# Kernel tuning notes

Hardware: AMD Instinct MI355X
Metric: run time of the kernel (lower is better)

## Reference

```python
import jax, jax.numpy as jnp
import numpy as np

B, L, C, H, FF = 2, 2048, 1024, 16, 4096
HD = C // H
SCALE = HD ** -0.5
EPS = 1e-5


def _ln(x, g, b):
    m = jnp.mean(x, axis=-1, keepdims=True)
    v = jnp.mean((x - m) ** 2, axis=-1, keepdims=True)
    return (x - m) * jax.lax.rsqrt(v + EPS) * g + b


def setup_inputs() -> dict:
    key = jax.random.key(0)
    ks = jax.random.split(key, 12)
    s = lambda fan_in: 1.0 / np.sqrt(fan_in)
    return {
        "x": jax.random.normal(ks[0], (B, L, C), jnp.float32),
        "freq_diff": jax.random.normal(ks[1], (B, L), jnp.float32),
        "qkv_w": jax.random.normal(ks[2], (C, 3 * C), jnp.float32) * s(C),
        "qkv_b": jnp.zeros((3 * C,), jnp.float32),
        "fp_w1": jax.random.normal(ks[3], (1, C), jnp.float32),
        "fp_b1": jnp.zeros((C,), jnp.float32),
        "fp_ln_g": jnp.ones((C,), jnp.float32),
        "fp_ln_b": jnp.zeros((C,), jnp.float32),
        "fp_w2": jax.random.normal(ks[4], (C, C), jnp.float32) * s(C),
        "fp_b2": jnp.zeros((C,), jnp.float32),
        "wq_w": jax.random.normal(ks[5], (HD, HD), jnp.float32) * s(HD),
        "wq_b": jnp.zeros((HD,), jnp.float32),
        "wk_w": jax.random.normal(ks[6], (HD, HD), jnp.float32) * s(HD),
        "wk_b": jnp.zeros((HD,), jnp.float32),
        "out_w": jax.random.normal(ks[7], (C, C), jnp.float32) * s(C),
        "out_b": jnp.zeros((C,), jnp.float32),
        "n1_g": jnp.ones((C,), jnp.float32),
        "n1_b": jnp.zeros((C,), jnp.float32),
        "n2_g": jnp.ones((C,), jnp.float32),
        "n2_b": jnp.zeros((C,), jnp.float32),
        "mlp_w1": jax.random.normal(ks[8], (C, FF), jnp.float32) * s(C),
        "mlp_b1": jnp.zeros((FF,), jnp.float32),
        "mlp_w2": jax.random.normal(ks[9], (FF, C), jnp.float32) * s(FF),
        "mlp_b2": jnp.zeros((C,), jnp.float32),
        "freq_scale": jnp.ones((1,), jnp.float32),
    }


def reference(x, freq_diff, qkv_w, qkv_b, fp_w1, fp_b1, fp_ln_g, fp_ln_b,
              fp_w2, fp_b2, wq_w, wq_b, wk_w, wk_b, out_w, out_b,
              n1_g, n1_b, n2_g, n2_b, mlp_w1, mlp_b1, mlp_w2, mlp_b2,
              freq_scale):
    shortcut = x
    xn = _ln(x, n1_g, n1_b)
    qkv = (xn @ qkv_w + qkv_b).reshape(B, L, 3, H, HD)
    qkv = jnp.transpose(qkv, (2, 0, 3, 1, 4))  # [3,B,H,L,HD]
    q, k, v = qkv[0], qkv[1], qkv[2]

    # frequency bias: MLP on scalar freq_diff -> per-head bias vectors
    fb = freq_diff[..., None] @ fp_w1 + fp_b1          # [B,L,C]
    fb = jax.nn.gelu(_ln(fb, fp_ln_g, fp_ln_b), approximate=False)
    fb = fb @ fp_w2 + fp_b2                            # [B,L,C]
    fb = jnp.transpose(fb.reshape(B, L, H, HD), (0, 2, 1, 3))  # [B,H,L,HD]
    qb = fb @ wq_w + wq_b
    kb = fb @ wk_w + wk_b
    freq_attn_bias = jnp.einsum('bhqd,bhkd->bhqk', qb, kb)

    attn = jnp.einsum('bhqd,bhkd->bhqk', q, k) * SCALE
    attn = attn + freq_scale[0] * freq_attn_bias
    attn = jax.nn.softmax(attn, axis=-1)
    o = jnp.einsum('bhqk,bhkd->bhqd', attn, v)
    o = jnp.transpose(o, (0, 2, 1, 3)).reshape(B, L, C)
    x = shortcut + (o @ out_w + out_b)

    xn2 = _ln(x, n2_g, n2_b)
    h = jax.nn.gelu(xn2 @ mlp_w1 + mlp_b1, approximate=False)
    x = x + (h @ mlp_w2 + mlp_b2)
    return x
```

## Files before the change

kernel.cpp:

```cpp
#include <hip/hip_runtime.h>
#include <math.h>


typedef __bf16 bf16;
typedef float f32x4 __attribute__((ext_vector_type(4)));
typedef bf16 bf16x8 __attribute__((ext_vector_type(8)));
typedef bf16 bf16x4 __attribute__((ext_vector_type(4)));

#define DEVINL __device__ __forceinline__

DEVINL void async_load16(const void* g, void* l) {
  __builtin_amdgcn_global_load_lds(
      (const __attribute__((address_space(1))) unsigned int*)g,
      (__attribute__((address_space(3))) unsigned int*)l, 16, 0, 0);
}

DEVINL f32x4 mfma16(bf16x8 a, bf16x8 b, f32x4 c) {
  return __builtin_amdgcn_mfma_f32_16x16x32_bf16(a, b, c, 0, 0, 0);
}

DEVINL float gelu_exact(float v) {
  return 0.5f * v * (1.0f + erff(v * 0.70710678118654752f));
}

DEVINL void block_reduce2(float& a, float& b, float* red, int tid) {
#pragma unroll
  for (int off = 32; off >= 1; off >>= 1) {
    a += __shfl_xor(a, off);
    b += __shfl_xor(b, off);
  }
  int w = tid >> 6;
  if ((tid & 63) == 0) { red[2 * w] = a; red[2 * w + 1] = b; }
  __syncthreads();
  a = red[0] + red[2] + red[4] + red[6];
  b = red[1] + red[3] + red[5] + red[7];
  __syncthreads();
}

__global__ __launch_bounds__(256) void transpose_cast(
    const float* __restrict__ W, bf16* __restrict__ Wt, int K, int N) {
  __shared__ float tile[32][33];
  int n0 = blockIdx.x * 32, k0 = blockIdx.y * 32;
  int tx = threadIdx.x & 31, ty = threadIdx.x >> 5;
#pragma unroll
  for (int r = 0; r < 4; ++r)
    tile[ty + r * 8][tx] = W[(size_t)(k0 + ty + r * 8) * N + n0 + tx];
  __syncthreads();
#pragma unroll
  for (int r = 0; r < 4; ++r)
    Wt[(size_t)(n0 + ty + r * 8) * K + k0 + tx] = (bf16)tile[tx][ty + r * 8];
}

__global__ __launch_bounds__(256) void prec_qk(
    const float* __restrict__ fp_w2, const float* __restrict__ fp_b2,
    const float* __restrict__ wq_w, const float* __restrict__ wq_b,
    const float* __restrict__ wk_w, const float* __restrict__ wk_b,
    bf16* __restrict__ wqk2t, float* __restrict__ bqk) {
  __shared__ float Wl[64 * 64];
  __shared__ float Al[64 * 128];
  const int id = blockIdx.x;
  const int sel = id >> 7, h = (id >> 3) & 15, ck = id & 7;
  const int t = threadIdx.x;
  const float* wsel = sel ? wk_w : wq_w;
#pragma unroll
  for (int i = 0; i < 4; ++i)
    ((float4*)Wl)[i * 256 + t] = ((const float4*)wsel)[i * 256 + t];
  const int c0 = ck * 128, off = h * 64;
#pragma unroll
  for (int it = 0; it < 8; ++it) {
    int idx = it * 256 + t;
    int rr = idx >> 4, c4 = idx & 15;
    float4 v = *(const float4*)(fp_w2 + (size_t)(c0 + rr) * 1024 + off + c4 * 4);
    float vv[4] = {v.x, v.y, v.z, v.w};
#pragma unroll
    for (int k = 0; k < 4; ++k) {
      int i2 = c4 * 4 + k;
      Al[i2 * 128 + (rr ^ (i2 & 31))] = vv[k];
    }
  }
  __syncthreads();
  const int cr = t & 127, jh = (t >> 7) * 32;
  float acc[32];
#pragma unroll
  for (int j = 0; j < 32; ++j) acc[j] = 0.f;
  for (int i = 0; i < 64; ++i) {
    float a = Al[i * 128 + (cr ^ (i & 31))];
    const float4* wrow = (const float4*)(Wl + i * 64 + jh);
#pragma unroll
    for (int j4 = 0; j4 < 8; ++j4) {
      float4 wv = wrow[j4];
      acc[j4 * 4 + 0] += a * wv.x;
      acc[j4 * 4 + 1] += a * wv.y;
      acc[j4 * 4 + 2] += a * wv.z;
      acc[j4 * 4 + 3] += a * wv.w;
    }
  }
  const int nbase = sel * 1024 + off + jh;
#pragma unroll
  for (int j = 0; j < 32; ++j)
    wqk2t[(size_t)(nbase + j) * 1024 + c0 + cr] = (bf16)acc[j];
  if (ck == 0 && t < 64) {
    float s = 0.f;
    for (int i = 0; i < 64; ++i) s += fp_b2[off + i] * Wl[i * 64 + t];
    bqk[sel * 1024 + off + t] = s + (sel ? wk_b[t] : wq_b[t]);
  }
}

__global__ __launch_bounds__(256) void ln1_kernel(
    const float* __restrict__ x, const float* __restrict__ fd,
    const float* __restrict__ g1, const float* __restrict__ b1,
    const float* __restrict__ fw1, const float* __restrict__ fb1,
    const float* __restrict__ flg, const float* __restrict__ flb,
    bf16* __restrict__ xn, bf16* __restrict__ gout) {
  __shared__ float red[8];
  int tok = blockIdx.x, t = threadIdx.x;
  float4 xv = ((const float4*)(x + (size_t)tok * 1024))[t];
  float s = xv.x + xv.y + xv.z + xv.w;
  float ss = xv.x * xv.x + xv.y * xv.y + xv.z * xv.z + xv.w * xv.w;
  block_reduce2(s, ss, red, t);
  float mean = s * (1.0f / 1024.0f);
  float rsig = rsqrtf(ss * (1.0f / 1024.0f) - mean * mean + 1e-5f);
  float4 g4 = ((const float4*)g1)[t], b4 = ((const float4*)b1)[t];
  bf16x4 o;
  o[0] = (bf16)((xv.x - mean) * rsig * g4.x + b4.x);
  o[1] = (bf16)((xv.y - mean) * rsig * g4.y + b4.y);
  o[2] = (bf16)((xv.z - mean) * rsig * g4.z + b4.z);
  o[3] = (bf16)((xv.w - mean) * rsig * g4.w + b4.w);
  ((bf16x4*)xn)[(size_t)tok * 256 + t] = o;

  float dv = fd[tok];
  float4 w4 = ((const float4*)fw1)[t], c4 = ((const float4*)fb1)[t];
  float f0 = dv * w4.x + c4.x, f1 = dv * w4.y + c4.y;
  float f2 = dv * w4.z + c4.z, f3 = dv * w4.w + c4.w;
  s = f0 + f1 + f2 + f3;
  ss = f0 * f0 + f1 * f1 + f2 * f2 + f3 * f3;
  block_reduce2(s, ss, red, t);
  mean = s * (1.0f / 1024.0f);
  rsig = rsqrtf(ss * (1.0f / 1024.0f) - mean * mean + 1e-5f);
  float4 lg = ((const float4*)flg)[t], lb = ((const float4*)flb)[t];
  bf16x4 q;
  q[0] = (bf16)gelu_exact((f0 - mean) * rsig * lg.x + lb.x);
  q[1] = (bf16)gelu_exact((f1 - mean) * rsig * lg.y + lb.y);
  q[2] = (bf16)gelu_exact((f2 - mean) * rsig * lg.z + lb.z);
  q[3] = (bf16)gelu_exact((f3 - mean) * rsig * lg.w + lb.w);
  ((bf16x4*)gout)[(size_t)tok * 256 + t] = q;
}

__global__ __launch_bounds__(256) void ln_kernel(
    const float* __restrict__ xin, const float* __restrict__ g,
    const float* __restrict__ b, bf16* __restrict__ xout) {
  __shared__ float red[8];
  int tok = blockIdx.x, t = threadIdx.x;
  float4 xv = ((const float4*)(xin + (size_t)tok * 1024))[t];
  float s = xv.x + xv.y + xv.z + xv.w;
  float ss = xv.x * xv.x + xv.y * xv.y + xv.z * xv.z + xv.w * xv.w;
  block_reduce2(s, ss, red, t);
  float mean = s * (1.0f / 1024.0f);
  float rsig = rsqrtf(ss * (1.0f / 1024.0f) - mean * mean + 1e-5f);
  float4 g4 = ((const float4*)g)[t], b4 = ((const float4*)b)[t];
  bf16x4 o;
  o[0] = (bf16)((xv.x - mean) * rsig * g4.x + b4.x);
  o[1] = (bf16)((xv.y - mean) * rsig * g4.y + b4.y);
  o[2] = (bf16)((xv.z - mean) * rsig * g4.z + b4.z);
  o[3] = (bf16)((xv.w - mean) * rsig * g4.w + b4.w);
  ((bf16x4*)xout)[(size_t)tok * 256 + t] = o;
}

template <class Epi>
__global__ __launch_bounds__(256) void gemm_bf16_k(
    const bf16* __restrict__ A, const bf16* __restrict__ Bt,
    int M, int N, int K, Epi epi) {
  __shared__ bf16 As[2][128 * 32];
  __shared__ bf16 Bs[2][128 * 32];
  const int tid = threadIdx.x;
  const int lane = tid & 63, w = tid >> 6;
  const int quad = lane >> 4, lm = lane & 15;
  const int wm = w >> 1, wn = w & 1;
  const int m0 = blockIdx.y * 128, n0 = blockIdx.x * 128;

  f32x4 acc[4][4];
#pragma unroll
  for (int i = 0; i < 4; ++i)
#pragma unroll
    for (int j = 0; j < 4; ++j) {
      acc[i][j][0] = 0.f; acc[i][j][1] = 0.f; acc[i][j][2] = 0.f; acc[i][j][3] = 0.f;
    }

  const bf16* Ag = A + (size_t)m0 * K;
  const bf16* Bg = Bt + (size_t)n0 * K;

  auto stage = [&](int k0, int buf) {
#pragma unroll
    for (int i = 0; i < 2; ++i) {
      int ch = i * 256 + tid, r = ch >> 2, c = ch & 3;
      async_load16(Ag + (size_t)r * K + k0 + c * 8,
                   (char*)As[buf] + (i * 256 + w * 64) * 16);
      async_load16(Bg + (size_t)r * K + k0 + c * 8,
                   (char*)Bs[buf] + (i * 256 + w * 64) * 16);
    }
  };

  stage(0, 0);
  const int nk = K >> 5;
  for (int ki = 0; ki < nk; ++ki) {
    __syncthreads();
    if (ki + 1 < nk) stage((ki + 1) << 5, (ki + 1) & 1);
    const bf16* Ac = As[ki & 1];
    const bf16* Bc = Bs[ki & 1];
    bf16x8 af[4], bfv[4];
#pragma unroll
    for (int mi = 0; mi < 4; ++mi)
      af[mi] = *(const bf16x8*)(Ac + (wm * 64 + mi * 16 + lm) * 32 + quad * 8);
#pragma unroll
    for (int ni = 0; ni < 4; ++ni)
      bfv[ni] = *(const bf16x8*)(Bc + (wn * 64 + ni * 16 + lm) * 32 + quad * 8);
#pragma unroll
    for (int mi = 0; mi < 4; ++mi)
#pragma unroll
      for (int ni = 0; ni < 4; ++ni)
        acc[mi][ni] = mfma16(af[mi], bfv[ni], acc[mi][ni]);
  }

#pragma unroll
  for (int mi = 0; mi < 4; ++mi)
#pragma unroll
    for (int ni = 0; ni < 4; ++ni)
      epi(m0 + wm * 64 + mi * 16 + quad * 4, n0 + wn * 64 + ni * 16 + lm, acc[mi][ni]);
}

__global__ __launch_bounds__(256) void gemm_mlp2_part(
    const bf16* __restrict__ A, const bf16* __restrict__ Bt,
    float* __restrict__ part) {
  __shared__ bf16 As[2][128 * 32];
  __shared__ bf16 Bs[2][128 * 32];
  const int tid = threadIdx.x;
  const int lane = tid & 63, w = tid >> 6;
  const int quad = lane >> 4, lm = lane & 15;
  const int wm = w >> 1, wn = w & 1;
  const int id = blockIdx.x;
  const int kz = id & 3;
  const int n0 = ((id >> 2) & 7) * 128;
  const int m0 = (id >> 5) * 128;

  f32x4 acc[4][4];
#pragma unroll
  for (int i = 0; i < 4; ++i)
#pragma unroll
    for (int j = 0; j < 4; ++j) {
      acc[i][j][0] = 0.f; acc[i][j][1] = 0.f; acc[i][j][2] = 0.f; acc[i][j][3] = 0.f;
    }

  const bf16* Ag = A + (size_t)m0 * 4096 + kz * 1024;
  const bf16* Bg = Bt + (size_t)n0 * 4096 + kz * 1024;

  auto stage = [&](int k0, int buf) {
#pragma unroll
    for (int i = 0; i < 2; ++i) {
      int ch = i * 256 + tid, r = ch >> 2, c = ch & 3;
      async_load16(Ag + (size_t)r * 4096 + k0 + c * 8,
                   (char*)As[buf] + (i * 256 + w * 64) * 16);
      async_load16(Bg + (size_t)r * 4096 + k0 + c * 8,
                   (char*)Bs[buf] + (i * 256 + w * 64) * 16);
    }
  };

  stage(0, 0);
  for (int ki = 0; ki < 32; ++ki) {
    __syncthreads();
    if (ki + 1 < 32) stage((ki + 1) << 5, (ki + 1) & 1);
    const bf16* Ac = As[ki & 1];
    const bf16* Bc = Bs[ki & 1];
    bf16x8 af[4], bfv[4];
#pragma unroll
    for (int mi = 0; mi < 4; ++mi)
      af[mi] = *(const bf16x8*)(Ac + (wm * 64 + mi * 16 + lm) * 32 + quad * 8);
#pragma unroll
    for (int ni = 0; ni < 4; ++ni)
      bfv[ni] = *(const bf16x8*)(Bc + (wn * 64 + ni * 16 + lm) * 32 + quad * 8);
#pragma unroll
    for (int mi = 0; mi < 4; ++mi)
#pragma unroll
      for (int ni = 0; ni < 4; ++ni)
        acc[mi][ni] = mfma16(af[mi], bfv[ni], acc[mi][ni]);
  }

  float* dst = part + (size_t)kz * 4096 * 1024;
#pragma unroll
  for (int mi = 0; mi < 4; ++mi)
#pragma unroll
    for (int ni = 0; ni < 4; ++ni) {
      int row = m0 + wm * 64 + mi * 16 + quad * 4;
      int col = n0 + wn * 64 + ni * 16 + lm;
#pragma unroll
      for (int r = 0; r < 4; ++r)
        dst[(size_t)(row + r) * 1024 + col] = acc[mi][ni][r];
    }
}

__global__ __launch_bounds__(256) void reduce_mlp2(
    const float* __restrict__ part, float* __restrict__ out) {
  size_t i = (size_t)blockIdx.x * 256 + threadIdx.x;
  const float4* p = (const float4*)part;
  float4 o = ((const float4*)out)[i];
  const size_t S = (size_t)4096 * 256;
  float4 a = p[i], b = p[i + S], c = p[i + 2 * S], d = p[i + 3 * S];
  o.x += a.x + b.x + c.x + d.x;
  o.y += a.y + b.y + c.y + d.y;
  o.z += a.z + b.z + c.z + d.z;
  o.w += a.w + b.w + c.w + d.w;
  ((float4*)out)[i] = o;
}

struct EpiQKV {
  const float* __restrict__ bias;
  bf16 *Qc, *Kc, *Vt;
  DEVINL void operator()(int row, int col, f32x4 v) const {
    int b = row >> 11, l = row & 2047;
    float bia = bias[col];
    if (col < 1024) {
      int h = col >> 6, d = col & 63;
      bf16* p = Qc + (size_t)(((b << 4) + h) * 2048 + l) * 128 + d;
#pragma unroll
      for (int r = 0; r < 4; ++r) p[r * 128] = (bf16)((v[r] + bia) * 0.125f);
    } else if (col < 2048) {
      int c2 = col - 1024, h = c2 >> 6, d = c2 & 63;
      bf16* p = Kc + (size_t)(((b << 4) + h) * 2048 + l) * 128 + d;
#pragma unroll
      for (int r = 0; r < 4; ++r) p[r * 128] = (bf16)(v[r] + bia);
    } else {
      int c2 = col - 2048, h = c2 >> 6, d = c2 & 63;
      bf16x4 pk;
#pragma unroll
      for (int r = 0; r < 4; ++r) pk[r] = (bf16)(v[r] + bia);
      *(bf16x4*)(Vt + (size_t)(((b << 4) + h) * 64 + d) * 2048 + l) = pk;
    }
  }
};

struct EpiQBKB {
  const float* __restrict__ bias;
  const float* __restrict__ fs;
  bf16 *Qc, *Kc;
  DEVINL void operator()(int row, int col, f32x4 v) const {
    int b = row >> 11, l = row & 2047;
    float bia = bias[col];
    if (col < 1024) {
      int h = col >> 6, d = col & 63;
      float sc = fs[0];
      bf16* p = Qc + (size_t)(((b << 4) + h) * 2048 + l) * 128 + 64 + d;
#pragma unroll
      for (int r = 0; r < 4; ++r) p[r * 128] = (bf16)((v[r] + bia) * sc);
    } else {
      int c2 = col - 1024, h = c2 >> 6, d = c2 & 63;
      bf16* p = Kc + (size_t)(((b << 4) + h) * 2048 + l) * 128 + 64 + d;
#pragma unroll
      for (int r = 0; r < 4; ++r) p[r * 128] = (bf16)(v[r] + bia);
    }
  }
};

struct EpiOut {
  const float* __restrict__ bias;
  const float* __restrict__ x;
  const float* __restrict__ b2;
  float* x1;
  float* out0;
  DEVINL void operator()(int row, int col, f32x4 v) const {
    float bia = bias[col];
    float b2v = b2[col];
#pragma unroll
    for (int r = 0; r < 4; ++r) {
      size_t idx = (size_t)(row + r) * 1024 + col;
      float xv = x[idx] + v[r] + bia;
      x1[idx] = xv;
      out0[idx] = xv + b2v;
    }
  }
};

struct EpiMLP1 {
  const float* __restrict__ bias;
  bf16* hbf;
  DEVINL void operator()(int row, int col, f32x4 v) const {
    float bia = bias[col];
#pragma unroll
    for (int r = 0; r < 4; ++r)
      hbf[(size_t)(row + r) * 4096 + col] = (bf16)gelu_exact(v[r] + bia);
  }
};

__global__ __launch_bounds__(256, 2) void flash_kernel(
    const bf16* __restrict__ Qc, const bf16* __restrict__ Kcp,
    const bf16* __restrict__ Vt, bf16* __restrict__ Obf) {
  __shared__ bf16 KsA[64 * 128];
  __shared__ bf16 KsB[64 * 128];
  __shared__ bf16 VsA[64 * 64];
  __shared__ bf16 VsB[64 * 64];
  __shared__ bf16 Ps[128 * 64];

  const int tid = threadIdx.x, lane = tid & 63, w = tid >> 6;
  const int quad = lane >> 4, lm = lane & 15;
  const int id = blockIdx.x;
  const int bh = id & 31, qt = id >> 5;
  const int b = bh >> 4, h = bh & 15;

  const bf16* Qg = Qc + ((size_t)bh * 2048 + qt * 128) * 128;
#pragma unroll
  for (int i = 0; i < 8; ++i) {
    int ch = i * 256 + tid, r = ch >> 4, cs = ch & 15, c = cs ^ (r & 7);
    char* dst = (r < 64) ? (char*)KsA + (i * 256 + w * 64) * 16
                         : (char*)KsB + ((i - 4) * 256 + w * 64) * 16;
    async_load16(Qg + (size_t)r * 128 + c * 8, dst);
  }
  __syncthreads();
  bf16x8 qf[2][4];
#pragma unroll
  for (int mi = 0; mi < 2; ++mi) {
    int r = w * 32 + mi * 16 + lm;
    const bf16* base = (r < 64) ? KsA : KsB;
#pragma unroll
    for (int ks = 0; ks < 4; ++ks) {
      int pos = (ks * 4 + quad) ^ (r & 7);
      qf[mi][ks] = *(const bf16x8*)(base + (r & 63) * 128 + pos * 8);
    }
  }
  __syncthreads();

  float m_run[2], l_run[2];
  f32x4 o_acc[2][4];
#pragma unroll
  for (int mi = 0; mi < 2; ++mi) { m_run[mi] = -3.0e38f; l_run[mi] = 0.f; }
#pragma unroll
  for (int mi = 0; mi < 2; ++mi)
#pragma unroll
    for (int nf = 0; nf < 4; ++nf) {
      o_acc[mi][nf][0] = 0.f; o_acc[mi][nf][1] = 0.f;
      o_acc[mi][nf][2] = 0.f; o_acc[mi][nf][3] = 0.f;
    }

  const bf16* Kg0 = Kcp + (size_t)bh * 2048 * 128;
  const bf16* Vg0 = Vt + (size_t)bh * 64 * 2048;

  auto stage = [&](int kv, bf16* Kdst, bf16* Vdst) {
    const bf16* Kg = Kg0 + (size_t)kv * 64 * 128;
#pragma unroll
    for (int i = 0; i < 4; ++i) {
      int ch = i * 256 + tid, key = ch >> 4, c = (ch & 15) ^ (key & 7);
      async_load16(Kg + (size_t)key * 128 + c * 8,
                   (char*)Kdst + (i * 256 + w * 64) * 16);
    }
#pragma unroll
    for (int i = 0; i < 2; ++i) {
      int ch = i * 256 + tid, d = ch >> 3, c = (ch & 7) ^ (d & 7);
      async_load16(Vg0 + (size_t)d * 2048 + kv * 64 + c * 8,
                   (char*)Vdst + (i * 256 + w * 64) * 16);
    }
  };

  stage(0, KsA, VsA);

  for (int kv = 0; kv < 32; ++kv) {
    const bf16* Kcur = (kv & 1) ? KsB : KsA;
    const bf16* Vcur = (kv & 1) ? VsB : VsA;
    __syncthreads();
    if (kv + 1 < 32)
      stage(kv + 1, (kv & 1) ? KsA : KsB, (kv & 1) ? VsA : VsB);

    f32x4 sa[2][4];
#pragma unroll
    for (int mi = 0; mi < 2; ++mi)
#pragma unroll
      for (int nk = 0; nk < 4; ++nk) {
        sa[mi][nk][0] = 0.f; sa[mi][nk][1] = 0.f;
        sa[mi][nk][2] = 0.f; sa[mi][nk][3] = 0.f;
      }
#pragma unroll
    for (int ks = 0; ks < 4; ++ks) {
      bf16x8 ak[4];
#pragma unroll
      for (int nk = 0; nk < 4; ++nk) {
        int key = nk * 16 + lm;
        int pos = (ks * 4 + quad) ^ (key & 7);
        ak[nk] = *(const bf16x8*)(Kcur + key * 128 + pos * 8);
      }
#pragma unroll
      for (int mi = 0; mi < 2; ++mi)
#pragma unroll
        for (int nk = 0; nk < 4; ++nk)
          sa[mi][nk] = mfma16(ak[nk], qf[mi][ks], sa[mi][nk]);
    }

    float al[2];
#pragma unroll
    for (int mi = 0; mi < 2; ++mi) {
      float mx = sa[mi][0][0];
#pragma unroll
      for (int nk = 0; nk < 4; ++nk)
#pragma unroll
        for (int rg = 0; rg < 4; ++rg) mx = fmaxf(mx, sa[mi][nk][rg]);
      mx = fmaxf(mx, __shfl_xor(mx, 16));
      mx = fmaxf(mx, __shfl_xor(mx, 32));
      float mnew = fmaxf(m_run[mi], mx);
      float a = __expf(m_run[mi] - mnew);
      m_run[mi] = mnew;
      al[mi] = a;
      float rs = 0.f;
#pragma unroll
      for (int nk = 0; nk < 4; ++nk)
#pragma unroll
        for (int rg = 0; rg < 4; ++rg) {
          float pv = __expf(sa[mi][nk][rg] - mnew);
          sa[mi][nk][rg] = pv;
          rs += pv;
        }
      rs += __shfl_xor(rs, 16);
      rs += __shfl_xor(rs, 32);
      l_run[mi] = l_run[mi] * a + rs;
    }

#pragma unroll
    for (int mi = 0; mi < 2; ++mi) {
#pragma unroll
      for (int rg = 0; rg < 4; ++rg) {
        float alr = __shfl(al[mi], quad * 4 + rg);
#pragma unroll
        for (int nf = 0; nf < 4; ++nf) o_acc[mi][nf][rg] *= alr;
      }
    }

#pragma unroll
    for (int mi = 0; mi < 2; ++mi) {
      int q = w * 32 + mi * 16 + lm;
#pragma unroll
      for (int nk = 0; nk < 4; ++nk) {
        int c8 = nk * 2 + (quad >> 1);
        int c8s = c8 ^ (q & 7);
        bf16x4 pk;
        pk[0] = (bf16)sa[mi][nk][0]; pk[1] = (bf16)sa[mi][nk][1];
        pk[2] = (bf16)sa[mi][nk][2]; pk[3] = (bf16)sa[mi][nk][3];
        *(bf16x4*)(Ps + q * 64 + c8s * 8 + (quad & 1) * 4) = pk;
      }
    }

#pragma unroll
    for (int ks = 0; ks < 2; ++ks) {
      bf16x8 pa[2], vb[4];
#pragma unroll
      for (int mi = 0; mi < 2; ++mi) {
        int q = w * 32 + mi * 16 + lm;
        int c8s = (ks * 4 + quad) ^ (q & 7);
        pa[mi] = *(const bf16x8*)(Ps + q * 64 + c8s * 8);
      }
#pragma unroll
      for (int nf = 0; nf < 4; ++nf) {
        int d = nf * 16 + lm;
        int c8s = (ks * 4 + quad) ^ (d & 7);
        vb[nf] = *(const bf16x8*)(Vcur + d * 64 + c8s * 8);
      }
#pragma unroll
      for (int mi = 0; mi < 2; ++mi)
#pragma unroll
        for (int nf = 0; nf < 4; ++nf)
          o_acc[mi][nf] = mfma16(pa[mi], vb[nf], o_acc[mi][nf]);
    }
  }

#pragma unroll
  for (int mi = 0; mi < 2; ++mi) {
#pragma unroll
    for (int rg = 0; rg < 4; ++rg) {
      float lr = __shfl(l_run[mi], quad * 4 + rg);
      float inv = 1.0f / lr;
      int l = qt * 128 + w * 32 + mi * 16 + quad * 4 + rg;
#pragma unroll
      for (int nf = 0; nf < 4; ++nf) {
        int d = h * 64 + nf * 16 + lm;
        Obf[((size_t)b * 2048 + l) * 1024 + d] = (bf16)(o_acc[mi][nf][rg] * inv);
      }
    }
  }
}

extern "C" void kernel_launch(void* const* d_in, const int* in_sizes, int n_in,
                              void* d_out, int out_size, void* d_ws, size_t ws_size,
                              hipStream_t stream) {
  (void)in_sizes; (void)n_in; (void)out_size; (void)ws_size;
  const float* x      = (const float*)d_in[0];
  const float* fd     = (const float*)d_in[1];
  const float* qkv_w  = (const float*)d_in[2];
  const float* qkv_b  = (const float*)d_in[3];
  const float* fp_w1  = (const float*)d_in[4];
  const float* fp_b1  = (const float*)d_in[5];
  const float* fp_ln_g= (const float*)d_in[6];
  const float* fp_ln_b= (const float*)d_in[7];
  const float* fp_w2  = (const float*)d_in[8];
  const float* fp_b2  = (const float*)d_in[9];
  const float* wq_w   = (const float*)d_in[10];
  const float* wq_b   = (const float*)d_in[11];
  const float* wk_w   = (const float*)d_in[12];
  const float* wk_b   = (const float*)d_in[13];
  const float* out_w  = (const float*)d_in[14];
  const float* out_b  = (const float*)d_in[15];
  const float* n1_g   = (const float*)d_in[16];
  const float* n1_b   = (const float*)d_in[17];
  const float* n2_g   = (const float*)d_in[18];
  const float* n2_b   = (const float*)d_in[19];
  const float* mlp_w1 = (const float*)d_in[20];
  const float* mlp_b1 = (const float*)d_in[21];
  const float* mlp_w2 = (const float*)d_in[22];
  const float* mlp_b2 = (const float*)d_in[23];
  const float* fscale = (const float*)d_in[24];
  float* out = (float*)d_out;

  char* p = (char*)d_ws;
  auto take = [&](size_t n) { char* r = p; p += (n + 255) & ~(size_t)255; return r; };
  bf16* xn_bf  = (bf16*)take((size_t)4096 * 1024 * 2);
  bf16* g_bf   = (bf16*)take((size_t)4096 * 1024 * 2);
  bf16* Qc     = (bf16*)take((size_t)32 * 2048 * 128 * 2);
  bf16* Kc     = (bf16*)take((size_t)32 * 2048 * 128 * 2);
  bf16* Vt     = (bf16*)take((size_t)32 * 64 * 2048 * 2);
  bf16* o_bf   = (bf16*)take((size_t)4096 * 1024 * 2);
  float* x1    = (float*)take((size_t)4096 * 1024 * 4);
  bf16* ln2_bf = (bf16*)take((size_t)4096 * 1024 * 2);
  bf16* h_bf   = (bf16*)take((size_t)4096 * 4096 * 2);
  bf16* qkv_wt = (bf16*)take((size_t)3072 * 1024 * 2);
  bf16* out_wt = (bf16*)take((size_t)1024 * 1024 * 2);
  bf16* w1t    = (bf16*)take((size_t)4096 * 1024 * 2);
  bf16* w2t    = (bf16*)take((size_t)1024 * 4096 * 2);
  bf16* wqk2t  = (bf16*)take((size_t)2048 * 1024 * 2);
  float* bqk   = (float*)take((size_t)2048 * 4);

  float* part = (float*)xn_bf;

  dim3 b256(256);

  transpose_cast<<<dim3(3072 / 32, 1024 / 32), b256, 0, stream>>>(qkv_w, qkv_wt, 1024, 3072);
  transpose_cast<<<dim3(1024 / 32, 1024 / 32), b256, 0, stream>>>(out_w, out_wt, 1024, 1024);
  transpose_cast<<<dim3(4096 / 32, 1024 / 32), b256, 0, stream>>>(mlp_w1, w1t, 1024, 4096);
  transpose_cast<<<dim3(1024 / 32, 4096 / 32), b256, 0, stream>>>(mlp_w2, w2t, 4096, 1024);
  prec_qk<<<dim3(256), b256, 0, stream>>>(fp_w2, fp_b2, wq_w, wq_b, wk_w, wk_b, wqk2t, bqk);

  ln1_kernel<<<dim3(4096), b256, 0, stream>>>(x, fd, n1_g, n1_b, fp_w1, fp_b1,
                                              fp_ln_g, fp_ln_b, xn_bf, g_bf);

  gemm_bf16_k<<<dim3(24, 32), b256, 0, stream>>>(xn_bf, qkv_wt, 4096, 3072, 1024,
                                                 EpiQKV{qkv_b, Qc, Kc, Vt});
  gemm_bf16_k<<<dim3(16, 32), b256, 0, stream>>>(g_bf, wqk2t, 4096, 2048, 1024,
                                                 EpiQBKB{bqk, fscale, Qc, Kc});
  flash_kernel<<<dim3(512), b256, 0, stream>>>(Qc, Kc, Vt, o_bf);

  gemm_bf16_k<<<dim3(8, 32), b256, 0, stream>>>(o_bf, out_wt, 4096, 1024, 1024,
                                                EpiOut{out_b, x, mlp_b2, x1, out});
  ln_kernel<<<dim3(4096), b256, 0, stream>>>(x1, n2_g, n2_b, ln2_bf);
  gemm_bf16_k<<<dim3(32, 32), b256, 0, stream>>>(ln2_bf, w1t, 4096, 4096, 1024,
                                                 EpiMLP1{mlp_b1, h_bf});
  gemm_mlp2_part<<<dim3(1024), b256, 0, stream>>>(h_bf, w2t, part);
  reduce_mlp2<<<dim3(4096), b256, 0, stream>>>(part, out);
}
```

Baseline: 496.1 us.

## Restructure flash attention to 512 threads with one query tile per wave

The flash kernel now uses 8 waves of 16 query rows each instead of 4 waves of 32 rows, which halves per-thread register state and the MFMA work per wave. Launch bounds go up to 512 threads so more waves can be resident. The PV product is reordered so each lane keeps its own row's statistics, which removes the alpha and l shuffles and allows vectorized output stores. Softmax now uses exp2, with log2(e) folded into the Q and bias scaling in the upstream epilogues. The cost is fewer MFMAs per LDS fragment load (less K/V reuse per wave) and possible register pressure under the tighter launch bounds.

```diff
diff --git a/kernel.cpp b/kernel.cpp
--- a/kernel.cpp
+++ b/kernel.cpp
@@ -8,6 +8,10 @@
 typedef bf16 bf16x4 __attribute__((ext_vector_type(4)));
 
 #define DEVINL __device__ __forceinline__
+
+#define LOG2E 1.4426950408889634f
+
+DEVINL float fast_exp2(float x) { return __builtin_amdgcn_exp2f(x); }
 
 DEVINL void async_load16(const void* g, void* l) {
   __builtin_amdgcn_global_load_lds(
@@ -321,7 +325,7 @@
       int h = col >> 6, d = col & 63;
       bf16* p = Qc + (size_t)(((b << 4) + h) * 2048 + l) * 128 + d;
 #pragma unroll
-      for (int r = 0; r < 4; ++r) p[r * 128] = (bf16)((v[r] + bia) * 0.125f);
+      for (int r = 0; r < 4; ++r) p[r * 128] = (bf16)((v[r] + bia) * (0.125f * LOG2E));
     } else if (col < 2048) {
       int c2 = col - 1024, h = c2 >> 6, d = c2 & 63;
       bf16* p = Kc + (size_t)(((b << 4) + h) * 2048 + l) * 128 + d;
@@ -346,7 +350,7 @@
     float bia = bias[col];
     if (col < 1024) {
       int h = col >> 6, d = col & 63;
-      float sc = fs[0];
+      float sc = fs[0] * LOG2E;
       bf16* p = Qc + (size_t)(((b << 4) + h) * 2048 + l) * 128 + 64 + d;
 #pragma unroll
       for (int r = 0; r < 4; ++r) p[r * 128] = (bf16)((v[r] + bia) * sc);
@@ -389,7 +393,7 @@
   }
 };
 
-__global__ __launch_bounds__(256, 2) void flash_kernel(
+__global__ __launch_bounds__(512, 4) void flash_kernel(
     const bf16* __restrict__ Qc, const bf16* __restrict__ Kcp,
     const bf16* __restrict__ Vt, bf16* __restrict__ Obf) {
   __shared__ bf16 KsA[64 * 128];
@@ -406,37 +410,32 @@
 
   const bf16* Qg = Qc + ((size_t)bh * 2048 + qt * 128) * 128;
 #pragma unroll
-  for (int i = 0; i < 8; ++i) {
-    int ch = i * 256 + tid, r = ch >> 4, cs = ch & 15, c = cs ^ (r & 7);
-    char* dst = (r < 64) ? (char*)KsA + (i * 256 + w * 64) * 16
-                         : (char*)KsB + ((i - 4) * 256 + w * 64) * 16;
+  for (int i = 0; i < 4; ++i) {
+    int ch = i * 512 + tid, r = ch >> 4, cs = ch & 15, c = cs ^ (r & 7);
+    char* dst = (i < 2) ? (char*)KsA + (i * 512 + w * 64) * 16
+                        : (char*)KsB + ((i - 2) * 512 + w * 64) * 16;
     async_load16(Qg + (size_t)r * 128 + c * 8, dst);
   }
   __syncthreads();
-  bf16x8 qf[2][4];
-#pragma unroll
-  for (int mi = 0; mi < 2; ++mi) {
-    int r = w * 32 + mi * 16 + lm;
-    const bf16* base = (r < 64) ? KsA : KsB;
+  const int qr = w * 16 + lm;
+  bf16x8 qf[4];
+  {
+    const bf16* base = (w < 4) ? KsA : KsB;
+    int rr = qr & 63;
 #pragma unroll
     for (int ks = 0; ks < 4; ++ks) {
-      int pos = (ks * 4 + quad) ^ (r & 7);
-      qf[mi][ks] = *(const bf16x8*)(base + (r & 63) * 128 + pos * 8);
+      int pos = (ks * 4 + quad) ^ (lm & 7);
+      qf[ks] = *(const bf16x8*)(base + rr * 128 + pos * 8);
     }
   }
   __syncthreads();
 
-  float m_run[2], l_run[2];
-  f32x4 o_acc[2][4];
-#pragma unroll
-  for (int mi = 0; mi < 2; ++mi) { m_run[mi] = -3.0e38f; l_run[mi] = 0.f; }
-#pragma unroll
-  for (int mi = 0; mi < 2; ++mi)
-#pragma unroll
-    for (int nf = 0; nf < 4; ++nf) {
-      o_acc[mi][nf][0] = 0.f; o_acc[mi][nf][1] = 0.f;
-      o_acc[mi][nf][2] = 0.f; o_acc[mi][nf][3] = 0.f;
-    }
+  float m_run = -3.0e38f, l_run = 0.f;
+  f32x4 o_acc[4];
+#pragma unroll
+  for (int nf = 0; nf < 4; ++nf) {
+    o_acc[nf][0] = 0.f; o_acc[nf][1] = 0.f; o_acc[nf][2] = 0.f; o_acc[nf][3] = 0.f;
+  }
 
   const bf16* Kg0 = Kcp + (size_t)bh * 2048 * 128;
   const bf16* Vg0 = Vt + (size_t)bh * 64 * 2048;
@@ -444,16 +443,15 @@
   auto stage = [&](int kv, bf16* Kdst, bf16* Vdst) {
     const bf16* Kg = Kg0 + (size_t)kv * 64 * 128;
 #pragma unroll
-    for (int i = 0; i < 4; ++i) {
-      int ch = i * 256 + tid, key = ch >> 4, c = (ch & 15) ^ (key & 7);
+    for (int i = 0; i < 2; ++i) {
+      int ch = i * 512 + tid, key = ch >> 4, c = (ch & 15) ^ (key & 7);
       async_load16(Kg + (size_t)key * 128 + c * 8,
-                   (char*)Kdst + (i * 256 + w * 64) * 16);
-    }
-#pragma unroll
-    for (int i = 0; i < 2; ++i) {
-      int ch = i * 256 + tid, d = ch >> 3, c = (ch & 7) ^ (d & 7);
+                   (char*)Kdst + (i * 512 + w * 64) * 16);
+    }
+    {
+      int d = tid >> 3, c = (tid & 7) ^ (d & 7);
       async_load16(Vg0 + (size_t)d * 2048 + kv * 64 + c * 8,
-                   (char*)Vdst + (i * 256 + w * 64) * 16);
+                   (char*)Vdst + (w * 64) * 16);
     }
   };
 
@@ -466,14 +464,11 @@
     if (kv + 1 < 32)
       stage(kv + 1, (kv & 1) ? KsA : KsB, (kv & 1) ? VsA : VsB);
 
-    f32x4 sa[2][4];
-#pragma unroll
-    for (int mi = 0; mi < 2; ++mi)
-#pragma unroll
-      for (int nk = 0; nk < 4; ++nk) {
-        sa[mi][nk][0] = 0.f; sa[mi][nk][1] = 0.f;
-        sa[mi][nk][2] = 0.f; sa[mi][nk][3] = 0.f;
-      }
+    f32x4 sa[4];
+#pragma unroll
+    for (int nk = 0; nk < 4; ++nk) {
+      sa[nk][0] = 0.f; sa[nk][1] = 0.f; sa[nk][2] = 0.f; sa[nk][3] = 0.f;
+    }
 #pragma unroll
     for (int ks = 0; ks < 4; ++ks) {
       bf16x8 ak[4];
@@ -484,100 +479,76 @@
         ak[nk] = *(const bf16x8*)(Kcur + key * 128 + pos * 8);
       }
 #pragma unroll
-      for (int mi = 0; mi < 2; ++mi)
-#pragma unroll
-        for (int nk = 0; nk < 4; ++nk)
-          sa[mi][nk] = mfma16(ak[nk], qf[mi][ks], sa[mi][nk]);
-    }
-
-    float al[2];
-#pragma unroll
-    for (int mi = 0; mi < 2; ++mi) {
-      float mx = sa[mi][0][0];
-#pragma unroll
       for (int nk = 0; nk < 4; ++nk)
-#pragma unroll
-        for (int rg = 0; rg < 4; ++rg) mx = fmaxf(mx, sa[mi][nk][rg]);
-      mx = fmaxf(mx, __shfl_xor(mx, 16));
-      mx = fmaxf(mx, __shfl_xor(mx, 32));
-      float mnew = fmaxf(m_run[mi], mx);
-      float a = __expf(m_run[mi] - mnew);
-      m_run[mi] = mnew;
-      al[mi] = a;
-      float rs = 0.f;
-#pragma unroll
-      for (int nk = 0; nk < 4; ++nk)
-#pragma unroll
-        for (int rg = 0; rg < 4; ++rg) {
-          float pv = __expf(sa[mi][nk][rg] - mnew);
-          sa[mi][nk][rg] = pv;
-          rs += pv;
-        }
-      rs += __shfl_xor(rs, 16);
-      rs += __shfl_xor(rs, 32);
-      l_run[mi] = l_run[mi] * a + rs;
-    }
-
-#pragma unroll
-    for (int mi = 0; mi < 2; ++mi) {
+        sa[nk] = mfma16(ak[nk], qf[ks], sa[nk]);
+    }
+
+    float mx = sa[0][0];
+#pragma unroll
+    for (int nk = 0; nk < 4; ++nk)
+#pragma unroll
+      for (int rg = 0; rg < 4; ++rg) mx = fmaxf(mx, sa[nk][rg]);
+    mx = fmaxf(mx, __shfl_xor(mx, 16));
+    mx = fmaxf(mx, __shfl_xor(mx, 32));
+    float mnew = fmaxf(m_run, mx);
+    float alpha = fast_exp2(m_run - mnew);
+    m_run = mnew;
+    float rs = 0.f;
+#pragma unroll
+    for (int nk = 0; nk < 4; ++nk)
 #pragma unroll
       for (int rg = 0; rg < 4; ++rg) {
-        float alr = __shfl(al[mi], quad * 4 + rg);
-#pragma unroll
-        for (int nf = 0; nf < 4; ++nf) o_acc[mi][nf][rg] *= alr;
+        float pv = fast_exp2(sa[nk][rg] - mnew);
+        sa[nk][rg] = pv;
+        rs += pv;
       }
-    }
-
-#pragma unroll
-    for (int mi = 0; mi < 2; ++mi) {
-      int q = w * 32 + mi * 16 + lm;
-#pragma unroll
-      for (int nk = 0; nk < 4; ++nk) {
-        int c8 = nk * 2 + (quad >> 1);
-        int c8s = c8 ^ (q & 7);
-        bf16x4 pk;
-        pk[0] = (bf16)sa[mi][nk][0]; pk[1] = (bf16)sa[mi][nk][1];
-        pk[2] = (bf16)sa[mi][nk][2]; pk[3] = (bf16)sa[mi][nk][3];
-        *(bf16x4*)(Ps + q * 64 + c8s * 8 + (quad & 1) * 4) = pk;
-      }
+    rs += __shfl_xor(rs, 16);
+    rs += __shfl_xor(rs, 32);
+    l_run = l_run * alpha + rs;
+#pragma unroll
+    for (int nf = 0; nf < 4; ++nf) {
+      o_acc[nf][0] *= alpha; o_acc[nf][1] *= alpha;
+      o_acc[nf][2] *= alpha; o_acc[nf][3] *= alpha;
+    }
+
+#pragma unroll
+    for (int nk = 0; nk < 4; ++nk) {
+      int c16 = 2 * nk + (quad >> 1);
+      int cs = c16 ^ (lm & 7);
+      bf16x4 pk;
+      pk[0] = (bf16)sa[nk][0]; pk[1] = (bf16)sa[nk][1];
+      pk[2] = (bf16)sa[nk][2]; pk[3] = (bf16)sa[nk][3];
+      *(bf16x4*)(Ps + qr * 64 + cs * 8 + (quad & 1) * 4) = pk;
     }
 
 #pragma unroll
     for (int ks = 0; ks < 2; ++ks) {
-      bf16x8 pa[2], vb[4];
-#pragma unroll
-      for (int mi = 0; mi < 2; ++mi) {
-        int q = w * 32 + mi * 16 + lm;
-        int c8s = (ks * 4 + quad) ^ (q & 7);
-        pa[mi] = *(const bf16x8*)(Ps + q * 64 + c8s * 8);
+      bf16x8 pa, vb[4];
+      {
+        int cs = (ks * 4 + quad) ^ (lm & 7);
+        pa = *(const bf16x8*)(Ps + qr * 64 + cs * 8);
       }
 #pragma unroll
       for (int nf = 0; nf < 4; ++nf) {
         int d = nf * 16 + lm;
-        int c8s = (ks * 4 + quad) ^ (d & 7);
-        vb[nf] = *(const bf16x8*)(Vcur + d * 64 + c8s * 8);
+        int cs = (ks * 4 + quad) ^ (d & 7);
+        vb[nf] = *(const bf16x8*)(Vcur + d * 64 + cs * 8);
       }
 #pragma unroll
-      for (int mi = 0; mi < 2; ++mi)
-#pragma unroll
-        for (int nf = 0; nf < 4; ++nf)
-          o_acc[mi][nf] = mfma16(pa[mi], vb[nf], o_acc[mi][nf]);
-    }
-  }
-
-#pragma unroll
-  for (int mi = 0; mi < 2; ++mi) {
-#pragma unroll
-    for (int rg = 0; rg < 4; ++rg) {
-      float lr = __shfl(l_run[mi], quad * 4 + rg);
-      float inv = 1.0f / lr;
-      int l = qt * 128 + w * 32 + mi * 16 + quad * 4 + rg;
-#pragma unroll
-      for (int nf = 0; nf < 4; ++nf) {
-        int d = h * 64 + nf * 16 + lm;
-        Obf[((size_t)b * 2048 + l) * 1024 + d] = (bf16)(o_acc[mi][nf][rg] * inv);
-      }
-    }
+      for (int nf = 0; nf < 4; ++nf)
+        o_acc[nf] = mfma16(vb[nf], pa, o_acc[nf]);
+    }
+  }
+
+  float inv = 1.0f / l_run;
+  int l = qt * 128 + qr;
+#pragma unroll
+  for (int nf = 0; nf < 4; ++nf) {
+    bf16x4 ov;
+#pragma unroll
+    for (int rg = 0; rg < 4; ++rg) ov[rg] = (bf16)(o_acc[nf][rg] * inv);
+    int d = h * 64 + nf * 16 + quad * 4;
+    *(bf16x4*)(Obf + ((size_t)b * 2048 + l) * 1024 + d) = ov;
   }
 }
 
@@ -647,7 +618,7 @@
                                                  EpiQKV{qkv_b, Qc, Kc, Vt});
   gemm_bf16_k<<<dim3(16, 32), b256, 0, stream>>>(g_bf, wqk2t, 4096, 2048, 1024,
                                                  EpiQBKB{bqk, fscale, Qc, Kc});
-  flash_kernel<<<dim3(512), b256, 0, stream>>>(Qc, Kc, Vt, o_bf);
+  flash_kernel<<<dim3(512), dim3(512), 0, stream>>>(Qc, Kc, Vt, o_bf);
 
   gemm_bf16_k<<<dim3(8, 32), b256, 0, stream>>>(o_bf, out_wt, 4096, 1024, 1024,
                                                 EpiOut{out_b, x, mlp_b2, x1, out});
```

Result: faster. 484.7 us (-2.3%).
